# Kernel optimization log

Hardware: AMD Instinct MI355X
Metric: run time of the kernel (lower is better)

Reference implementation:

```python
import jax, jax.numpy as jnp
import numpy as np

B, T, E, H = 8, 2048, 256, 8
D = E // H  # head_size = 32
EPS = 1e-5  # torch LayerNorm default


def _layernorm(x, g, b):
    m = jnp.mean(x, axis=-1, keepdims=True)
    v = jnp.var(x, axis=-1, keepdims=True)
    return (x - m) / jnp.sqrt(v + EPS) * g + b


def setup_inputs() -> dict:
    key = jax.random.key(0)
    ks = jax.random.split(key, 9)
    s = lambda k, shape, fan: (jax.random.normal(k, shape, jnp.float32) / np.sqrt(fan)).astype(jnp.float32)
    return {
        "x": jax.random.normal(ks[0], (B, T, E), jnp.float32),
        "wq": s(ks[1], (H, E, D), E),
        "wk": s(ks[2], (H, E, D), E),
        "wv": s(ks[3], (H, E, D), E),
        "w_lin": s(ks[4], (E, E), E),
        "b_lin": jnp.zeros((E,), jnp.float32),
        "g1": jnp.ones((E,), jnp.float32),
        "beta1": jnp.zeros((E,), jnp.float32),
        "g2": jnp.ones((E,), jnp.float32),
        "beta2": jnp.zeros((E,), jnp.float32),
        "w_f1": s(ks[5], (E, 4 * E), E),
        "b_f1": jnp.zeros((4 * E,), jnp.float32),
        "w_f2": s(ks[6], (4 * E, E), 4 * E),
        "b_f2": jnp.zeros((E,), jnp.float32),
    }


def reference(x, wq, wk, wv, w_lin, b_lin, g1, beta1, g2, beta2, w_f1, b_f1, w_f2, b_f2):
    b, t, e = x.shape
    xn = _layernorm(x, g1, beta1)  # norm1
    # all heads at once: (B,T,E) x (H,E,D) -> (B,H,T,D)
    q = jnp.einsum('bte,hed->bhtd', xn, wq)
    k = jnp.einsum('bte,hed->bhtd', xn, wk)
    v = jnp.einsum('bte,hed->bhtd', xn, wv)
    # scale uses C = embedding_size (as in source, not head_size)
    scores = jnp.einsum('bhtd,bhsd->bhts', q, k) * (e ** -0.5)
    mask = jnp.tril(jnp.ones((t, t), bool))  # (query t, key s)
    scores = jnp.where(mask[None, None, :, :], scores, -jnp.inf)
    # source applies softmax over dim=1 of (B,T,T) = the QUERY axis -> axis 2 of bhts
    attn = jax.nn.softmax(scores, axis=2)
    heads = jnp.einsum('bhts,bhsd->bhtd', attn, v)
    heads = heads.transpose(0, 2, 1, 3).reshape(b, t, e)  # concat over heads
    xh = xn + heads  # residual around attention
    xl = xh @ w_lin + b_lin  # projection (dropout is identity at eval)
    x2 = _layernorm(xl, g2, beta2)  # norm2
    ff = jax.nn.relu(x2 @ w_f1 + b_f1) @ w_f2 + b_f2  # FFN (dropout identity)
    return x2 + ff
```

## Files before the change

### kernel.cpp

```cpp
#include <hip/hip_runtime.h>
#include <math.h>

#define TT 2048
#define TE 256
#define NTOK 16384
#define QSCALE (0.0625f * 1.44269504088896f)

typedef short  bf16x8 __attribute__((ext_vector_type(8)));
typedef float  f32x4  __attribute__((ext_vector_type(4)));
typedef float  f32x16 __attribute__((ext_vector_type(16)));
typedef unsigned short u16x4 __attribute__((ext_vector_type(4)));
typedef unsigned short u16x8 __attribute__((ext_vector_type(8)));

__device__ __forceinline__ unsigned short f2b(float f) {
    union { float f; unsigned int u; } v; v.f = f;
    unsigned int r = v.u + 0x7FFF + ((v.u >> 16) & 1);
    return (unsigned short)(r >> 16);
}
__device__ __forceinline__ float b2f(unsigned short u) {
    union { unsigned int i; float f; } v; v.i = ((unsigned int)u) << 16;
    return v.f;
}
#if __has_builtin(__builtin_amdgcn_cvt_pk_bf16_f32)
__device__ __forceinline__ unsigned int pk_bf16(float a, float b) {
    typedef __bf16 bf2 __attribute__((ext_vector_type(2)));
    union { bf2 v; unsigned int u; } u;
    u.v = __builtin_amdgcn_cvt_pk_bf16_f32(a, b);
    return u.u;
}
#else
__device__ __forceinline__ unsigned int pk_bf16(float a, float b) {
    return (unsigned int)f2b(a) | ((unsigned int)f2b(b) << 16);
}
#endif
#if __has_builtin(__builtin_amdgcn_exp2f)
#define FEXP2(x) __builtin_amdgcn_exp2f(x)
#else
#define FEXP2(x) __expf(0.69314718056f * (x))
#endif
__device__ __forceinline__ void pswap(unsigned &a, unsigned &b) {
#if __has_builtin(__builtin_amdgcn_permlane32_swap)
    auto r = __builtin_amdgcn_permlane32_swap(a, b, false, false);
    a = r[0]; b = r[1];
#else
    asm("v_permlane32_swap_b32 %0, %1" : "+v"(a), "+v"(b));
#endif
}
__device__ __forceinline__ bf16x8 ld8(const unsigned short* p) {
    return *(const bf16x8*)p;
}
__device__ __forceinline__ void gl_lds16(const unsigned short* g, unsigned short* l) {
    __builtin_amdgcn_global_load_lds(
        (const __attribute__((address_space(1))) unsigned int*)(uintptr_t)g,
        (__attribute__((address_space(3))) unsigned int*)(uintptr_t)l,
        16, 0, 0);
}
#define MFMA16(a, b, c) __builtin_amdgcn_mfma_f32_16x16x32_bf16((a), (b), (c), 0, 0, 0)
#define MFMA32(a, b, c) __builtin_amdgcn_mfma_f32_32x32x16_bf16((a), (b), (c), 0, 0, 0)
#define SETPRIO(n) __builtin_amdgcn_s_setprio(n)


__device__ __forceinline__ void soft_pv(const f32x16 st, bf16x8 vv0, bf16x8 vv1,
                                        bool diag, int hi, int l31, f32x16& acc) {
    unsigned Wd[8];
    if (diag) {
#pragma unroll
        for (int j = 0; j < 8; ++j) {
            int r0 = 2 * j;
            int s0 = (r0 & 3) + 8 * (r0 >> 2) + 4 * hi;
            float e0 = (s0 <= l31)     ? FEXP2(st[r0])     : 0.f;
            float e1 = (s0 + 1 <= l31) ? FEXP2(st[r0 + 1]) : 0.f;
            Wd[j] = pk_bf16(e0, e1);
        }
    } else {
#pragma unroll
        for (int j = 0; j < 8; ++j)
            Wd[j] = pk_bf16(FEXP2(st[2 * j]), FEXP2(st[2 * j + 1]));
    }
    pswap(Wd[0], Wd[2]); pswap(Wd[1], Wd[3]);
    pswap(Wd[4], Wd[6]); pswap(Wd[5], Wd[7]);
    union { unsigned u4[4]; bf16x8 v; } pa0, pa1;
    pa0.u4[0] = Wd[0]; pa0.u4[1] = Wd[1]; pa0.u4[2] = Wd[2]; pa0.u4[3] = Wd[3];
    pa1.u4[0] = Wd[4]; pa1.u4[1] = Wd[5]; pa1.u4[2] = Wd[6]; pa1.u4[3] = Wd[7];
    SETPRIO(1);
    acc = MFMA32(pa0.v, vv0, acc);
    acc = MFMA32(pa1.v, vv1, acc);
    SETPRIO(0);
}

__device__ __forceinline__ void accum_exp(const f32x16 st, bool diag,
                                          int hi, int l31, float* acc) {
    if (diag) {
#pragma unroll
        for (int r = 0; r < 16; ++r) {
            int s_local = (r & 3) + 8 * (r >> 2) + 4 * hi;
            acc[r] += (l31 >= s_local) ? FEXP2(st[r]) : 0.f;
        }
    } else {
#pragma unroll
        for (int r = 0; r < 16; ++r) acc[r] += FEXP2(st[r]);
    }
}

__global__ __launch_bounds__(256) void prep(const float* __restrict__ wq,
                                            const float* __restrict__ wk,
                                            const float* __restrict__ wv,
                                            const float* __restrict__ w_lin,
                                            const float* __restrict__ w_f1,
                                            const float* __restrict__ w_f2,
                                            unsigned short* __restrict__ Wqkv,
                                            unsigned short* __restrict__ Wlin,
                                            unsigned short* __restrict__ Wf1,
                                            unsigned short* __restrict__ Wf2,
                                            const float* __restrict__ X,
                                            const float* __restrict__ g,
                                            const float* __restrict__ bta,
                                            unsigned short* __restrict__ Yb) {
    if (blockIdx.x >= 3072) {
        int row = (blockIdx.x - 3072) * 4 + (threadIdx.x >> 6);
        int lane = threadIdx.x & 63;
        const float4 v = *(const float4*)&X[(size_t)row * TE + lane * 4];
        float s = v.x + v.y + v.z + v.w;
        float s2 = v.x * v.x + v.y * v.y + v.z * v.z + v.w * v.w;
#pragma unroll
        for (int off = 1; off <= 32; off <<= 1) {
            s  += __shfl_xor(s,  off, 64);
            s2 += __shfl_xor(s2, off, 64);
        }
        float mean = s * (1.0f / TE);
        float var = s2 * (1.0f / TE) - mean * mean;
        float rstd = rsqrtf(var + 1e-5f);
        const float4 gg = *(const float4*)&g[lane * 4];
        const float4 bb = *(const float4*)&bta[lane * 4];
        u16x4 ob = { f2b((v.x - mean) * rstd * gg.x + bb.x),
                     f2b((v.y - mean) * rstd * gg.y + bb.y),
                     f2b((v.z - mean) * rstd * gg.z + bb.z),
                     f2b((v.w - mean) * rstd * gg.w + bb.w) };
        *(u16x4*)&Yb[(size_t)row * TE + lane * 4] = ob;
        return;
    }
    int idx = blockIdx.x * 256 + threadIdx.x;
    if (idx < 196608) {
        int n = idx >> 8, k = idx & 255;
        int which = n >> 8, h = (n >> 5) & 7, d = n & 31;
        const float* w = (which == 0) ? wq : (which == 1) ? wk : wv;
        Wqkv[idx] = f2b(w[(h * 256 + k) * 32 + d]);
    } else if (idx < 262144) {
        int i = idx - 196608; int n = i >> 8, k = i & 255;
        Wlin[i] = f2b(w_lin[k * 256 + n]);
    } else if (idx < 524288) {
        int i = idx - 262144; int n = i >> 8, k = i & 255;
        Wf1[i] = f2b(w_f1[k * 1024 + n]);
    } else {
        int i = idx - 524288; int n = i >> 10, k = i & 1023;
        Wf2[i] = f2b(w_f2[k * 256 + n]);
    }
}

__global__ __launch_bounds__(256) void ln2_red(const float* __restrict__ Pp,
                                               const float* __restrict__ bias,
                                               const float* __restrict__ g,
                                               const float* __restrict__ bta,
                                               unsigned short* __restrict__ Yb) {
    const size_t SL = (size_t)NTOK * TE;
    int row = blockIdx.x * 4 + (threadIdx.x >> 6);
    int lane = threadIdx.x & 63;
    size_t base = (size_t)row * TE + lane * 4;
    const float4 p0 = *(const float4*)&Pp[base];
    const float4 p1 = *(const float4*)&Pp[SL + base];
    const float4 bl = *(const float4*)&bias[lane * 4];
    float4 v;
    v.x = p0.x + p1.x + bl.x; v.y = p0.y + p1.y + bl.y;
    v.z = p0.z + p1.z + bl.z; v.w = p0.w + p1.w + bl.w;
    float s = v.x + v.y + v.z + v.w;
    float s2 = v.x * v.x + v.y * v.y + v.z * v.z + v.w * v.w;
#pragma unroll
    for (int off = 1; off <= 32; off <<= 1) {
        s  += __shfl_xor(s,  off, 64);
        s2 += __shfl_xor(s2, off, 64);
    }
    float mean = s * (1.0f / TE);
    float var = s2 * (1.0f / TE) - mean * mean;
    float rstd = rsqrtf(var + 1e-5f);
    const float4 gg = *(const float4*)&g[lane * 4];
    const float4 bb = *(const float4*)&bta[lane * 4];
    u16x4 ob = { f2b((v.x - mean) * rstd * gg.x + bb.x),
                 f2b((v.y - mean) * rstd * gg.y + bb.y),
                 f2b((v.z - mean) * rstd * gg.z + bb.z),
                 f2b((v.w - mean) * rstd * gg.w + bb.w) };
    *(u16x4*)&Yb[base] = ob;
}

__global__ __launch_bounds__(256) void reduce2(const unsigned short* __restrict__ Pf,
                                               const float* __restrict__ bias,
                                               const unsigned short* __restrict__ x2b,
                                               float* __restrict__ out) {
    const size_t SL = (size_t)NTOK * TE;
    int row = blockIdx.x * 4 + (threadIdx.x >> 6);
    int lane = threadIdx.x & 63;
    size_t base = (size_t)row * TE + lane * 4;
    const float4 bl = *(const float4*)&bias[lane * 4];
    u16x4 r = *(const u16x4*)&x2b[base];
    float4 acc;
    acc.x = bl.x + b2f(r[0]); acc.y = bl.y + b2f(r[1]);
    acc.z = bl.z + b2f(r[2]); acc.w = bl.w + b2f(r[3]);
#pragma unroll
    for (int z = 0; z < 4; ++z) {
        u16x4 p = *(const u16x4*)&Pf[z * SL + base];
        acc.x += b2f(p[0]); acc.y += b2f(p[1]);
        acc.z += b2f(p[2]); acc.w += b2f(p[3]);
    }
    *(float4*)&out[base] = acc;
}

template<int KS>
__global__ __launch_bounds__(256) void gemm_lds(const unsigned short* __restrict__ A,
                                                int lda,
                                                const unsigned short* __restrict__ Bt,
                                                int ldb,
                                                const float* __restrict__ bias,
                                                float* __restrict__ outF,
                                                unsigned short* __restrict__ outB,
                                                int N, int relu) {
    __shared__ unsigned short Al[3][128 * 32];
    __shared__ unsigned short Bl[3][128 * 32];
    int tid = threadIdx.x;
    int w = tid >> 6, lane = tid & 63, q = lane >> 4, col = lane & 15;
    int wm = w & 1, wn = w >> 1;
    int m0 = blockIdx.x * 128;
    int n0 = blockIdx.y * 128;
    int koff = blockIdx.z * KS;
    size_t zoff = (size_t)blockIdx.z * NTOK * N;
    f32x4 acc[4][4] = {};
    int srow = lane >> 2;
    int skq  = ((lane & 3) ^ ((srow >> 1) & 3)) * 8;
    const unsigned short* Ag0 = A  + (size_t)(m0 + w * 32 + srow) * lda + koff + skq;
    const unsigned short* Ag1 = Ag0 + (size_t)16 * lda;
    const unsigned short* Bg0 = Bt + (size_t)(n0 + w * 32 + srow) * ldb + koff + skq;
    const unsigned short* Bg1 = Bg0 + (size_t)16 * ldb;
    int rq = (q ^ ((col >> 1) & 3)) * 8;
#define G_STAGE(bf, kk) do { \
        gl_lds16(Ag0 + (kk), &Al[bf][(w * 32) * 32]); \
        gl_lds16(Ag1 + (kk), &Al[bf][(w * 32 + 16) * 32]); \
        gl_lds16(Bg0 + (kk), &Bl[bf][(w * 32) * 32]); \
        gl_lds16(Bg1 + (kk), &Bl[bf][(w * 32 + 16) * 32]); \
    } while (0)
    G_STAGE(0, 0);
    G_STAGE(1, 32);
#pragma unroll
    for (int k0 = 0; k0 < KS; k0 += 32) {
        const int jb = (k0 >> 5) % 3;
        if (k0 + 32 < KS) { asm volatile("s_waitcnt vmcnt(4)" ::: "memory"); }
        else              { asm volatile("s_waitcnt vmcnt(0)" ::: "memory"); }
        __builtin_amdgcn_s_barrier();
        if (k0 + 64 < KS) G_STAGE((jb + 2) % 3, k0 + 64);
        bf16x8 a[4], b[4];
#pragma unroll
        for (int i = 0; i < 4; ++i)
            a[i] = ld8(&Al[jb][(wm * 64 + i * 16 + col) * 32 + rq]);
#pragma unroll
        for (int j = 0; j < 4; ++j)
            b[j] = ld8(&Bl[jb][(wn * 64 + j * 16 + col) * 32 + rq]);
#pragma unroll
        for (int i = 0; i < 4; ++i)
#pragma unroll
            for (int j = 0; j < 4; ++j)
                acc[i][j] = MFMA16(a[i], b[j], acc[i][j]);
        __builtin_amdgcn_sched_barrier(0);
    }
#undef G_STAGE
    float* Cb = (float*)&Al[0][0];
    const int CLD = 132;
#pragma unroll
    for (int i = 0; i < 4; ++i) {
        __syncthreads();
#pragma unroll
        for (int j = 0; j < 4; ++j)
#pragma unroll
            for (int r = 0; r < 4; ++r)
                Cb[(wm * 16 + q * 4 + r) * CLD + wn * 64 + j * 16 + col] = acc[i][j][r];
        __syncthreads();
        int row = tid >> 3;
        int seg = (tid & 7) * 16;
        int mloc = (row & 15) + i * 16 + (row >> 4) * 64;
        int m = m0 + mloc;
        int n = n0 + seg;
        float vbuf[16];
#pragma unroll
        for (int u = 0; u < 16; ++u) vbuf[u] = Cb[row * CLD + seg + u];
        if (bias) {
#pragma unroll
            for (int u4 = 0; u4 < 4; ++u4) {
                float4 bb = *(const float4*)&bias[n + u4 * 4];
                vbuf[u4 * 4 + 0] += bb.x; vbuf[u4 * 4 + 1] += bb.y;
                vbuf[u4 * 4 + 2] += bb.z; vbuf[u4 * 4 + 3] += bb.w;
            }
        }
        if (relu) {
#pragma unroll
            for (int u = 0; u < 16; ++u) vbuf[u] = fmaxf(vbuf[u], 0.f);
        }
        if (outF) {
#pragma unroll
            for (int u = 0; u < 16; u += 4)
                *(float4*)&outF[zoff + (size_t)m * N + n + u] = *(const float4*)&vbuf[u];
        }
        if (outB) {
            u16x8 o0, o1;
#pragma unroll
            for (int u = 0; u < 8; ++u) { o0[u] = f2b(vbuf[u]); o1[u] = f2b(vbuf[8 + u]); }
            *(u16x8*)&outB[zoff + (size_t)m * N + n] = o0;
            *(u16x8*)&outB[zoff + (size_t)m * N + n + 8] = o1;
        }
    }
}

__global__ __launch_bounds__(256) void gemm_qkv(const unsigned short* __restrict__ A,
                                                const unsigned short* __restrict__ Bt,
                                                unsigned short* __restrict__ Qd,
                                                unsigned short* __restrict__ Kd,
                                                unsigned short* __restrict__ Vc) {
    const int K = 256;
    __shared__ unsigned short Al[3][128 * 32];
    __shared__ unsigned short Bl[3][128 * 32];
    int tid = threadIdx.x;
    int w = tid >> 6, lane = tid & 63, q = lane >> 4, col = lane & 15;
    int wm = w & 1, wn = w >> 1;
    int m0 = blockIdx.x * 128;
    int n0 = blockIdx.y * 128;
    f32x4 acc[4][4] = {};
    int srow = lane >> 2;
    int skq  = ((lane & 3) ^ ((srow >> 1) & 3)) * 8;
    const unsigned short* Ag0 = A  + (size_t)(m0 + w * 32 + srow) * K + skq;
    const unsigned short* Ag1 = Ag0 + (size_t)16 * K;
    const unsigned short* Bg0 = Bt + (size_t)(n0 + w * 32 + srow) * K + skq;
    const unsigned short* Bg1 = Bg0 + (size_t)16 * K;
    int rq = (q ^ ((col >> 1) & 3)) * 8;
#define G_STAGE(bf, kk) do { \
        gl_lds16(Ag0 + (kk), &Al[bf][(w * 32) * 32]); \
        gl_lds16(Ag1 + (kk), &Al[bf][(w * 32 + 16) * 32]); \
        gl_lds16(Bg0 + (kk), &Bl[bf][(w * 32) * 32]); \
        gl_lds16(Bg1 + (kk), &Bl[bf][(w * 32 + 16) * 32]); \
    } while (0)
    G_STAGE(0, 0);
    G_STAGE(1, 32);
#pragma unroll
    for (int k0 = 0; k0 < K; k0 += 32) {
        const int jb = (k0 >> 5) % 3;
        if (k0 + 32 < K) { asm volatile("s_waitcnt vmcnt(4)" ::: "memory"); }
        else             { asm volatile("s_waitcnt vmcnt(0)" ::: "memory"); }
        __builtin_amdgcn_s_barrier();
        if (k0 + 64 < K) G_STAGE((jb + 2) % 3, k0 + 64);
        bf16x8 a[4], b[4];
#pragma unroll
        for (int i = 0; i < 4; ++i)
            a[i] = ld8(&Al[jb][(wm * 64 + i * 16 + col) * 32 + rq]);
#pragma unroll
        for (int j = 0; j < 4; ++j)
            b[j] = ld8(&Bl[jb][(wn * 64 + j * 16 + col) * 32 + rq]);
#pragma unroll
        for (int i = 0; i < 4; ++i)
#pragma unroll
            for (int j = 0; j < 4; ++j)
                acc[i][j] = MFMA16(a[i], b[j], acc[i][j]);
        __builtin_amdgcn_sched_barrier(0);
    }
#undef G_STAGE
#pragma unroll
    for (int i = 0; i < 4; ++i)
#pragma unroll
    for (int j = 0; j < 4; ++j) {
        int n = n0 + wn * 64 + j * 16 + col;
        int which = n >> 8, h = (n >> 5) & 7, d = n & 31;
        int m = m0 + wm * 64 + i * 16 + q * 4;
        int b = m >> 11, t = m & 2047;
        int bh = b * 8 + h;
        if (which == 0) {
            size_t qb = ((size_t)(bh * 2 + (d >> 4)) * TT + t) * 16 + (d & 15);
#pragma unroll
            for (int r = 0; r < 4; ++r)
                Qd[qb + r * 16] = f2b(acc[i][j][r] * QSCALE);
        } else if (which == 1) {
            size_t kb = ((size_t)(bh * 2 + (d >> 4)) * TT + t) * 16 + (d & 15);
#pragma unroll
            for (int r = 0; r < 4; ++r)
                Kd[kb + r * 16] = f2b(acc[i][j][r]);
        } else {
            uint2 pv;
            pv.x = pk_bf16(acc[i][j][0], acc[i][j][1]);
            pv.y = pk_bf16(acc[i][j][2], acc[i][j][3]);
            *(uint2*)&Vc[(((size_t)bh * 256 + (t >> 3)) * 32 + d) * 8 + (t & 7)] = pv;
        }
    }
}

__global__ __launch_bounds__(256, 2) void attn_cols(const unsigned short* __restrict__ Qd,
                                                    const unsigned short* __restrict__ Kd,
                                                    unsigned short* __restrict__ Vc) {
    __shared__ float Lb[4][32];
    __shared__ float Linv[32];
    int tid = threadIdx.x;
    int w = tid >> 6, lane = tid & 63, hi = lane >> 5, l31 = lane & 31;
    int bh = blockIdx.x;
    int u = blockIdx.y;
    const unsigned short* Qb = Qd + ((size_t)bh * 2 * TT + l31) * 16 + hi * 8;
    const unsigned short* Kb = Kd + ((size_t)bh * 2 * TT + l31) * 16 + hi * 8;
    const f32x16 z16 = {};
#pragma unroll
    for (int phase = 0; phase < 2; ++phase) {
        int stile = phase ? (63 - u) : u;
        int sbase = stile * 32;
        bf16x8 a0 = ld8(Kb + (size_t)sbase * 16);
        bf16x8 a1 = ld8(Kb + ((size_t)TT + sbase) * 16);
        float acc[16] = {};
        int c = stile + w;
        bool diagP = (w == 0);
        bf16x8 qP0, qP1, qQ0, qQ1;
        if (c < 64) {
            qP0 = ld8(Qb + (size_t)(c * 32) * 16);
            qP1 = ld8(Qb + ((size_t)TT + c * 32) * 16);
        }
        if (c + 4 < 64) {
            qQ0 = ld8(Qb + (size_t)((c + 4) * 32) * 16);
            qQ1 = ld8(Qb + ((size_t)TT + (c + 4) * 32) * 16);
        }
        while (c + 8 < 64) {
            SETPRIO(1);
            f32x16 stP = MFMA32(a0, qP0, z16); stP = MFMA32(a1, qP1, stP);
            SETPRIO(0);
            qP0 = ld8(Qb + (size_t)((c + 8) * 32) * 16);
            qP1 = ld8(Qb + ((size_t)TT + (c + 8) * 32) * 16);
            SETPRIO(1);
            f32x16 stQ = MFMA32(a0, qQ0, z16); stQ = MFMA32(a1, qQ1, stQ);
            SETPRIO(0);
            accum_exp(stP, diagP, hi, l31, acc); diagP = false;
            if (c + 12 < 64) {
                qQ0 = ld8(Qb + (size_t)((c + 12) * 32) * 16);
                qQ1 = ld8(Qb + ((size_t)TT + (c + 12) * 32) * 16);
            }
            accum_exp(stQ, false, hi, l31, acc);
            c += 8;
        }
        if (c < 64) {
            f32x16 stP = MFMA32(a0, qP0, z16); stP = MFMA32(a1, qP1, stP);
            accum_exp(stP, diagP, hi, l31, acc);
        }
        if (c + 4 < 64) {
            f32x16 stQ = MFMA32(a0, qQ0, z16); stQ = MFMA32(a1, qQ1, stQ);
            accum_exp(stQ, false, hi, l31, acc);
        }
#pragma unroll
        for (int off = 1; off <= 16; off <<= 1)
#pragma unroll
            for (int r = 0; r < 16; ++r) acc[r] += __shfl_xor(acc[r], off, 64);
        if (l31 == 0) {
#pragma unroll
            for (int r = 0; r < 16; ++r) {
                int s_local = (r & 3) + 8 * (r >> 2) + 4 * hi;
                Lb[w][s_local] = acc[r];
            }
        }
        __syncthreads();
        if (tid < 32)
            Linv[tid] = 1.0f / (Lb[0][tid] + Lb[1][tid] + Lb[2][tid] + Lb[3][tid]);
        __syncthreads();
        if (tid < 128) {
            int sbl = tid >> 5;
            int d = tid & 31;
            size_t base = (((size_t)bh * 256 + stile * 4 + sbl) * 32 + d) * 8;
            u16x8 v = *(const u16x8*)&Vc[base];
            u16x8 o;
#pragma unroll
            for (int e = 0; e < 8; ++e) o[e] = f2b(b2f(v[e]) * Linv[sbl * 8 + e]);
            *(u16x8*)&Vc[base] = o;
        }
        __syncthreads();
    }
}

__global__ __launch_bounds__(256, 2) void attn_out(const unsigned short* __restrict__ Qd,
                                                   const unsigned short* __restrict__ Kd,
                                                   const unsigned short* __restrict__ Vc,
                                                   const unsigned short* __restrict__ xnb,
                                                   unsigned short* __restrict__ xh_bf) {
    __shared__ float Ob[4][16][36];
    int tid = threadIdx.x;
    int w = tid >> 6, lane = tid & 63, hi = lane >> 5, l31 = lane & 31;
    int bh = blockIdx.x, b = bh >> 3, h = bh & 7;
    int u = blockIdx.y;
    const unsigned short* Kb = Kd + ((size_t)bh * 2 * TT + l31) * 16 + hi * 8;
    const unsigned short* Vb = Vc + (size_t)bh * 65536 + hi * 256 + l31 * 8;
    const unsigned short* Qbase = Qd + ((size_t)bh * 2 * TT + l31) * 16 + hi * 8;
    const f32x16 z16 = {};

#pragma unroll
    for (int phase = 0; phase < 2; ++phase) {
        int tt = phase ? (63 - u) : u;
        int tbase = tt * 32;
        bf16x8 q0 = ld8(Qbase + (size_t)tbase * 16);
        bf16x8 q1 = ld8(Qbase + ((size_t)TT + tbase) * 16);
        f32x16 acc = z16;

        int c = w;
        bf16x8 kP0, kP1, vP0, vP1, kQ0, kQ1, vQ0, vQ1;
        if (c <= tt) {
            kP0 = ld8(Kb + (size_t)c * 512);
            kP1 = ld8(Kb + (size_t)TT * 16 + (size_t)c * 512);
            vP0 = ld8(Vb + (size_t)c * 1024);
            vP1 = ld8(Vb + (size_t)c * 1024 + 512);
        }
        if (c + 4 <= tt) {
            kQ0 = ld8(Kb + (size_t)(c + 4) * 512);
            kQ1 = ld8(Kb + (size_t)TT * 16 + (size_t)(c + 4) * 512);
            vQ0 = ld8(Vb + (size_t)(c + 4) * 1024);
            vQ1 = ld8(Vb + (size_t)(c + 4) * 1024 + 512);
        }
        while (c + 8 <= tt) {
            SETPRIO(1);
            f32x16 stP = MFMA32(kP0, q0, z16); stP = MFMA32(kP1, q1, stP);
            SETPRIO(0);
            kP0 = ld8(Kb + (size_t)(c + 8) * 512);
            kP1 = ld8(Kb + (size_t)TT * 16 + (size_t)(c + 8) * 512);
            SETPRIO(1);
            f32x16 stQ = MFMA32(kQ0, q0, z16); stQ = MFMA32(kQ1, q1, stQ);
            SETPRIO(0);
            soft_pv(stP, vP0, vP1, false, hi, l31, acc);
            vP0 = ld8(Vb + (size_t)(c + 8) * 1024);
            vP1 = ld8(Vb + (size_t)(c + 8) * 1024 + 512);
            if (c + 12 <= tt) {
                kQ0 = ld8(Kb + (size_t)(c + 12) * 512);
                kQ1 = ld8(Kb + (size_t)TT * 16 + (size_t)(c + 12) * 512);
            }
            soft_pv(stQ, vQ0, vQ1, false, hi, l31, acc);
            if (c + 12 <= tt) {
                vQ0 = ld8(Vb + (size_t)(c + 12) * 1024);
                vQ1 = ld8(Vb + (size_t)(c + 12) * 1024 + 512);
            }
            c += 8;
        }
        if (c <= tt) {
            f32x16 stP = MFMA32(kP0, q0, z16); stP = MFMA32(kP1, q1, stP);
            soft_pv(stP, vP0, vP1, c == tt, hi, l31, acc);
        }
        if (c + 4 <= tt) {
            f32x16 stQ = MFMA32(kQ0, q0, z16); stQ = MFMA32(kQ1, q1, stQ);
            soft_pv(stQ, vQ0, vQ1, c + 4 == tt, hi, l31, acc);
        }

#pragma unroll
        for (int half = 0; half < 2; ++half) {
#pragma unroll
            for (int rr = 0; rr < 8; ++rr) {
                int r = half * 8 + rr;
                int t16 = (r & 3) + 8 * ((r >> 2) & 1) + 4 * hi;
                Ob[w][t16][l31] = acc[r];
            }
            __syncthreads();
            if (tid < 128) {
                int row = tid >> 3;
                int c4 = (tid & 7) * 4;
                float4 s0 = *(const float4*)&Ob[0][row][c4];
                float4 s1 = *(const float4*)&Ob[1][row][c4];
                float4 s2 = *(const float4*)&Ob[2][row][c4];
                float4 s3 = *(const float4*)&Ob[3][row][c4];
                size_t base = ((size_t)(b * TT) + tbase + half * 16 + row) * TE
                              + h * 32 + c4;
                u16x4 xv = *(const u16x4*)&xnb[base];
                u16x4 ob = { f2b(s0.x + s1.x + s2.x + s3.x + b2f(xv[0])),
                             f2b(s0.y + s1.y + s2.y + s3.y + b2f(xv[1])),
                             f2b(s0.z + s1.z + s2.z + s3.z + b2f(xv[2])),
                             f2b(s0.w + s1.w + s2.w + s3.w + b2f(xv[3])) };
                *(u16x4*)&xh_bf[base] = ob;
            }
            __syncthreads();
        }
    }
}

extern "C" void kernel_launch(void* const* d_in, const int* in_sizes, int n_in,
                              void* d_out, int out_size, void* d_ws, size_t ws_size,
                              hipStream_t stream) {
    (void)in_sizes; (void)n_in; (void)out_size; (void)ws_size;
    const float* x     = (const float*)d_in[0];
    const float* wq    = (const float*)d_in[1];
    const float* wk    = (const float*)d_in[2];
    const float* wv    = (const float*)d_in[3];
    const float* w_lin = (const float*)d_in[4];
    const float* b_lin = (const float*)d_in[5];
    const float* g1    = (const float*)d_in[6];
    const float* beta1 = (const float*)d_in[7];
    const float* g2    = (const float*)d_in[8];
    const float* beta2 = (const float*)d_in[9];
    const float* w_f1  = (const float*)d_in[10];
    const float* b_f1  = (const float*)d_in[11];
    const float* w_f2  = (const float*)d_in[12];
    const float* b_f2  = (const float*)d_in[13];
    float* out = (float*)d_out;

    char* ws = (char*)d_ws;
    unsigned short* Wqkv_t = (unsigned short*)(ws + 0);
    unsigned short* Wlin_t = (unsigned short*)(ws + 393216);
    unsigned short* Wf1_t  = (unsigned short*)(ws + 524288);
    unsigned short* Wf2_t  = (unsigned short*)(ws + 1048576);
    unsigned short* xn_bf  = (unsigned short*)(ws + 2097152);
    unsigned short* Qbf    = (unsigned short*)(ws + 10485760);
    unsigned short* Kbf    = (unsigned short*)(ws + 18874368);
    unsigned short* Vt     = (unsigned short*)(ws + 27262976);
    unsigned short* xh_bf  = (unsigned short*)(ws + 35651584);
    float*          Pp     = (float*)(ws + 44040192);
    unsigned short* Pf     = (unsigned short*)(ws + 44040192);
    unsigned short* x2_bf  = xn_bf;
    unsigned short* h_bf   = Qbf;

    prep<<<7168, 256, 0, stream>>>(wq, wk, wv, w_lin, w_f1, w_f2,
                                   Wqkv_t, Wlin_t, Wf1_t, Wf2_t,
                                   x, g1, beta1, xn_bf);
    gemm_qkv<<<dim3(128, 6), 256, 0, stream>>>(xn_bf, Wqkv_t, Qbf, Kbf, Vt);
    attn_cols<<<dim3(64, 32), 256, 0, stream>>>(Qbf, Kbf, Vt);
    attn_out<<<dim3(64, 32), 256, 0, stream>>>(Qbf, Kbf, Vt, xn_bf, xh_bf);
    gemm_lds<128><<<dim3(128, 2, 2), 256, 0, stream>>>(xh_bf, 256, Wlin_t, 256,
                                                       nullptr, Pp, nullptr, 256, 0);
    ln2_red<<<4096, 256, 0, stream>>>(Pp, b_lin, g2, beta2, x2_bf);
    gemm_lds<256><<<dim3(128, 8, 1), 256, 0, stream>>>(x2_bf, 256, Wf1_t, 256,
                                                       b_f1, nullptr, h_bf, 1024, 1);
    gemm_lds<256><<<dim3(128, 2, 4), 256, 0, stream>>>(h_bf, 1024, Wf2_t, 1024,
                                                       nullptr, nullptr, Pf, 256, 0);
    reduce2<<<4096, 256, 0, stream>>>(Pf, b_f2, x2_bf, out);
}
```

Before: 240.5 us.

## Drop split-K in projection and FFN2 GEMMs; fuse bias and residual epilogue

Removes the split-K partitioning from the projection and second FFN GEMMs so each block covers the full K range and writes final results directly. The FFN2 GEMM epilogue now adds bias and the bf16 residual and writes fp32 output, which eliminates the reduce2 kernel and the partial-sum traffic. ln2_red now reads a single partial. The trade-off is fewer blocks (256 instead of 512/1024) with longer K loops, which lowers parallelism on a large-CU device.

Result: faster. 225.4 us (-6.3%).

```diff
diff --git a/kernel.cpp b/kernel.cpp
--- a/kernel.cpp
+++ b/kernel.cpp
@@ -162,16 +162,14 @@
                                                const float* __restrict__ g,
                                                const float* __restrict__ bta,
                                                unsigned short* __restrict__ Yb) {
-    const size_t SL = (size_t)NTOK * TE;
     int row = blockIdx.x * 4 + (threadIdx.x >> 6);
     int lane = threadIdx.x & 63;
     size_t base = (size_t)row * TE + lane * 4;
     const float4 p0 = *(const float4*)&Pp[base];
-    const float4 p1 = *(const float4*)&Pp[SL + base];
     const float4 bl = *(const float4*)&bias[lane * 4];
     float4 v;
-    v.x = p0.x + p1.x + bl.x; v.y = p0.y + p1.y + bl.y;
-    v.z = p0.z + p1.z + bl.z; v.w = p0.w + p1.w + bl.w;
+    v.x = p0.x + bl.x; v.y = p0.y + bl.y;
+    v.z = p0.z + bl.z; v.w = p0.w + bl.w;
     float s = v.x + v.y + v.z + v.w;
     float s2 = v.x * v.x + v.y * v.y + v.z * v.z + v.w * v.w;
 #pragma unroll
@@ -191,34 +189,13 @@
     *(u16x4*)&Yb[base] = ob;
 }
 
-__global__ __launch_bounds__(256) void reduce2(const unsigned short* __restrict__ Pf,
-                                               const float* __restrict__ bias,
-                                               const unsigned short* __restrict__ x2b,
-                                               float* __restrict__ out) {
-    const size_t SL = (size_t)NTOK * TE;
-    int row = blockIdx.x * 4 + (threadIdx.x >> 6);
-    int lane = threadIdx.x & 63;
-    size_t base = (size_t)row * TE + lane * 4;
-    const float4 bl = *(const float4*)&bias[lane * 4];
-    u16x4 r = *(const u16x4*)&x2b[base];
-    float4 acc;
-    acc.x = bl.x + b2f(r[0]); acc.y = bl.y + b2f(r[1]);
-    acc.z = bl.z + b2f(r[2]); acc.w = bl.w + b2f(r[3]);
-#pragma unroll
-    for (int z = 0; z < 4; ++z) {
-        u16x4 p = *(const u16x4*)&Pf[z * SL + base];
-        acc.x += b2f(p[0]); acc.y += b2f(p[1]);
-        acc.z += b2f(p[2]); acc.w += b2f(p[3]);
-    }
-    *(float4*)&out[base] = acc;
-}
-
 template<int KS>
 __global__ __launch_bounds__(256) void gemm_lds(const unsigned short* __restrict__ A,
                                                 int lda,
                                                 const unsigned short* __restrict__ Bt,
                                                 int ldb,
                                                 const float* __restrict__ bias,
+                                                const unsigned short* __restrict__ resid,
                                                 float* __restrict__ outF,
                                                 unsigned short* __restrict__ outB,
                                                 int N, int relu) {
@@ -229,14 +206,12 @@
     int wm = w & 1, wn = w >> 1;
     int m0 = blockIdx.x * 128;
     int n0 = blockIdx.y * 128;
-    int koff = blockIdx.z * KS;
-    size_t zoff = (size_t)blockIdx.z * NTOK * N;
     f32x4 acc[4][4] = {};
     int srow = lane >> 2;
     int skq  = ((lane & 3) ^ ((srow >> 1) & 3)) * 8;
-    const unsigned short* Ag0 = A  + (size_t)(m0 + w * 32 + srow) * lda + koff + skq;
+    const unsigned short* Ag0 = A  + (size_t)(m0 + w * 32 + srow) * lda + skq;
     const unsigned short* Ag1 = Ag0 + (size_t)16 * lda;
-    const unsigned short* Bg0 = Bt + (size_t)(n0 + w * 32 + srow) * ldb + koff + skq;
+    const unsigned short* Bg0 = Bt + (size_t)(n0 + w * 32 + srow) * ldb + skq;
     const unsigned short* Bg1 = Bg0 + (size_t)16 * ldb;
     int rq = (q ^ ((col >> 1) & 3)) * 8;
 #define G_STAGE(bf, kk) do { \
@@ -296,6 +271,15 @@
                 vbuf[u4 * 4 + 2] += bb.z; vbuf[u4 * 4 + 3] += bb.w;
             }
         }
+        if (resid) {
+            u16x8 r0 = *(const u16x8*)&resid[(size_t)m * N + n];
+            u16x8 r1 = *(const u16x8*)&resid[(size_t)m * N + n + 8];
+#pragma unroll
+            for (int u = 0; u < 8; ++u) {
+                vbuf[u]     += b2f(r0[u]);
+                vbuf[8 + u] += b2f(r1[u]);
+            }
+        }
         if (relu) {
 #pragma unroll
             for (int u = 0; u < 16; ++u) vbuf[u] = fmaxf(vbuf[u], 0.f);
@@ -303,14 +287,14 @@
         if (outF) {
 #pragma unroll
             for (int u = 0; u < 16; u += 4)
-                *(float4*)&outF[zoff + (size_t)m * N + n + u] = *(const float4*)&vbuf[u];
+                *(float4*)&outF[(size_t)m * N + n + u] = *(const float4*)&vbuf[u];
         }
         if (outB) {
             u16x8 o0, o1;
 #pragma unroll
             for (int u = 0; u < 8; ++u) { o0[u] = f2b(vbuf[u]); o1[u] = f2b(vbuf[8 + u]); }
-            *(u16x8*)&outB[zoff + (size_t)m * N + n] = o0;
-            *(u16x8*)&outB[zoff + (size_t)m * N + n + 8] = o1;
+            *(u16x8*)&outB[(size_t)m * N + n] = o0;
+            *(u16x8*)&outB[(size_t)m * N + n + 8] = o1;
         }
     }
 }
@@ -608,7 +592,6 @@
     unsigned short* Vt     = (unsigned short*)(ws + 27262976);
     unsigned short* xh_bf  = (unsigned short*)(ws + 35651584);
     float*          Pp     = (float*)(ws + 44040192);
-    unsigned short* Pf     = (unsigned short*)(ws + 44040192);
     unsigned short* x2_bf  = xn_bf;
     unsigned short* h_bf   = Qbf;
 
@@ -618,12 +601,11 @@
     gemm_qkv<<<dim3(128, 6), 256, 0, stream>>>(xn_bf, Wqkv_t, Qbf, Kbf, Vt);
     attn_cols<<<dim3(64, 32), 256, 0, stream>>>(Qbf, Kbf, Vt);
     attn_out<<<dim3(64, 32), 256, 0, stream>>>(Qbf, Kbf, Vt, xn_bf, xh_bf);
-    gemm_lds<128><<<dim3(128, 2, 2), 256, 0, stream>>>(xh_bf, 256, Wlin_t, 256,
-                                                       nullptr, Pp, nullptr, 256, 0);
+    gemm_lds<256><<<dim3(128, 2), 256, 0, stream>>>(xh_bf, 256, Wlin_t, 256,
+                                                    nullptr, nullptr, Pp, nullptr, 256, 0);
     ln2_red<<<4096, 256, 0, stream>>>(Pp, b_lin, g2, beta2, x2_bf);
-    gemm_lds<256><<<dim3(128, 8, 1), 256, 0, stream>>>(x2_bf, 256, Wf1_t, 256,
-                                                       b_f1, nullptr, h_bf, 1024, 1);
-    gemm_lds<256><<<dim3(128, 2, 4), 256, 0, stream>>>(h_bf, 1024, Wf2_t, 1024,
-                                                       nullptr, nullptr, Pf, 256, 0);
-    reduce2<<<4096, 256, 0, stream>>>(Pf, b_f2, x2_bf, out);
-}
+    gemm_lds<256><<<dim3(128, 8), 256, 0, stream>>>(x2_bf, 256, Wf1_t, 256,
+                                                    b_f1, nullptr, nullptr, h_bf, 1024, 1);
+    gemm_lds<1024><<<dim3(128, 2), 256, 0, stream>>>(h_bf, 1024, Wf2_t, 1024,
+                                                     b_f2, x2_bf, out, nullptr, 256, 0);
+}
```
